# Kernel optimization log

Measured on AMD Instinct MI355X. Metric: run time of the kernel, lower is better.

## Reference

```python
import jax, jax.numpy as jnp
import numpy as np

N_NODES = 10000
N_EDGES = 640000
D_FEAT = 128
EPS = 1e-12  # F.normalize default eps


def setup_inputs() -> dict:
    key = jax.random.key(0)
    k1, k2, k3 = jax.random.split(key, 3)
    x = jax.random.normal(k1, (N_NODES, D_FEAT), dtype=jnp.float32)
    edge = jax.random.randint(k2, (3, N_EDGES), 0, N_NODES, dtype=jnp.int64)
    edge_weight = jax.random.uniform(k3, (N_EDGES,), dtype=jnp.float32)
    return {"x": x, "edge": edge, "edge_weight": edge_weight}


def reference(x, edge, edge_weight):
    edge_j = edge[0]  # source nodes
    edge_i = edge[2]  # target nodes
    n = x.shape[0]
    # degree of each target node (scatter_add of edge weights)
    deg = jax.ops.segment_sum(edge_weight, edge_i, num_segments=n)
    # normalized edge weights: w_e = ew_e / deg[target(e)]
    w = edge_weight / deg[edge_i]
    # SpMM: out[i] = sum_{e: target=i} w_e * x[source(e)]
    msg = x[edge_j] * w[:, None]           # [E, D]
    out = jax.ops.segment_sum(msg, edge_i, num_segments=n)  # [N, D]
    out = jax.nn.relu(out)
    # row-wise L2 normalize (F.normalize: x / max(||x||, eps))
    norm = jnp.sqrt(jnp.sum(out * out, axis=1, keepdims=True))
    return out / jnp.maximum(norm, EPS)
```

## Files before the change

kernel.cpp:

```cpp
#include <hip/hip_runtime.h>
#include <hip/hip_fp16.h>
#include <math.h>

#define D_FEAT 128
#define EPS 1e-12f
#define TGRP 40
#define NBUCK_PAD 256
#define NBLK 250
#define CAP_CB 40
#define SLOTS_PB (NBLK * CAP_CB)
#define LCAP 3584


__device__ inline float2 h2_to_f2(unsigned int u) {
    __half2 h = *reinterpret_cast<__half2*>(&u);
    return __half22float2(h);
}

__global__ __launch_bounds__(1024)
void build_kernel(const int* __restrict__ edge_i,
                  const int* __restrict__ edge_j,
                  const float* __restrict__ ew,
                  const float* __restrict__ x,
                  unsigned int* __restrict__ xh,
                  unsigned char* __restrict__ cntcb,
                  uint2* __restrict__ payload,
                  int E, int total4, int nbuck) {
    __shared__ unsigned int hc[NBUCK_PAD];
    const int c   = blockIdx.x;
    const int tid = threadIdx.x;
    const int EPB = E / NBLK;

    if (tid < NBUCK_PAD) hc[tid] = 0;
    __syncthreads();

    for (int i = c * 1024 + tid; i < total4; i += NBLK * 1024) {
        float4 v = ((const float4*)x)[i];
        __half2 h01 = __floats2half2_rn(v.x, v.y);
        __half2 h23 = __floats2half2_rn(v.z, v.w);
        uint2 o;
        o.x = *reinterpret_cast<unsigned int*>(&h01);
        o.y = *reinterpret_cast<unsigned int*>(&h23);
        ((uint2*)xh)[i] = o;
    }

    const int e0 = c * EPB;
    for (int k = tid; k < EPB; k += 1024) {
        int e = e0 + k;
        int t = edge_i[e];
        int bkt  = t / TGRP;
        int tloc = t - bkt * TGRP;
        unsigned int r = atomicAdd(&hc[bkt], 1u);
        if (r < CAP_CB) {
            unsigned short hw = __half_as_ushort(__float2half(ew[e]));
            payload[(size_t)bkt * SLOTS_PB + c * CAP_CB + r] =
                make_uint2(((unsigned int)edge_j[e] << 16) | (unsigned int)hw,
                           (unsigned int)tloc);
        }
    }
    __syncthreads();

    if (tid < nbuck) {
        unsigned int v = hc[tid];
        cntcb[(size_t)tid * NBUCK_PAD + c] =
            (unsigned char)(v > CAP_CB ? CAP_CB : v);
    }
}

__global__ __launch_bounds__(1024)
void sort_gather_kernel(const unsigned char* __restrict__ cntcb,
                        const uint2* __restrict__ payload,
                        const unsigned int* __restrict__ xh,
                        float* __restrict__ out, int n) {
    __shared__ unsigned char  cnt_c[NBLK];
    __shared__ unsigned int   cnt40[TGRP];
    __shared__ unsigned int   base40[TGRP + 1];
    __shared__ unsigned short rank16[SLOTS_PB];
    __shared__ unsigned int   ssw[LCAP];
    const int b   = blockIdx.x;
    const int tid = threadIdx.x;
    const int wv   = tid >> 6;
    const int lane = tid & 63;
    const int g    = lane >> 4;
    const int l16  = lane & 15;

    if (tid < NBLK) cnt_c[tid] = cntcb[(size_t)b * NBUCK_PAD + tid];
    if (tid < TGRP) cnt40[tid] = 0;
    __syncthreads();

    const uint2* __restrict__ pb = payload + (size_t)b * SLOTS_PB;

    for (int s = tid; s < SLOTS_PB; s += 1024) {
        uint2 pl = pb[s];
        int c = s / CAP_CB;
        int k = s - c * CAP_CB;
        if (k < (int)cnt_c[c]) {
            unsigned int r = atomicAdd(&cnt40[pl.y], 1u);
            rank16[s] = (unsigned short)r;
        }
    }
    __syncthreads();

    if (tid == 0) {
        unsigned int run = 0;
        for (int t = 0; t < TGRP; ++t) { base40[t] = run; run += cnt40[t]; }
        base40[TGRP] = run;
    }
    __syncthreads();

    for (int s = tid; s < SLOTS_PB; s += 1024) {
        uint2 pl = pb[s];
        int c = s / CAP_CB;
        int k = s - c * CAP_CB;
        if (k < (int)cnt_c[c]) {
            unsigned int pos = base40[pl.y] + (unsigned int)rank16[s];
            if (pos < LCAP) ssw[pos] = pl.x;
        }
    }
    __syncthreads();

    const uint4* __restrict__ xr = (const uint4*)xh;
    for (int tl = wv; tl < TGRP; tl += 16) {
        int t = b * TGRP + tl;
        if (t >= n) break;
        int beg = (int)base40[tl];
        int m   = (int)cnt40[tl];
        if (beg + m > LCAP) m = (LCAP - beg > 0) ? (LCAP - beg) : 0;

        float4 accA = {0.f,0.f,0.f,0.f};
        float4 accB = {0.f,0.f,0.f,0.f};

        int it = 0;
        for (; it + 15 < m; it += 16) {
            unsigned int pq[4]; uint4 hq[4];
            #pragma unroll
            for (int q = 0; q < 4; ++q) pq[q] = ssw[beg + it + q * 4 + g];
            #pragma unroll
            for (int q = 0; q < 4; ++q) hq[q] = xr[(size_t)(pq[q] >> 16) * 16 + l16];
            #pragma unroll
            for (int q = 0; q < 4; ++q) {
                float w = __half2float(__ushort_as_half((unsigned short)(pq[q] & 0xffffu)));
                float2 f;
                f = h2_to_f2(hq[q].x); accA.x = fmaf(f.x, w, accA.x); accA.y = fmaf(f.y, w, accA.y);
                f = h2_to_f2(hq[q].y); accA.z = fmaf(f.x, w, accA.z); accA.w = fmaf(f.y, w, accA.w);
                f = h2_to_f2(hq[q].z); accB.x = fmaf(f.x, w, accB.x); accB.y = fmaf(f.y, w, accB.y);
                f = h2_to_f2(hq[q].w); accB.z = fmaf(f.x, w, accB.z); accB.w = fmaf(f.y, w, accB.w);
            }
        }
        for (; it < m; it += 4) {
            int idx = it + g;
            unsigned int p = (idx < m) ? ssw[beg + idx] : 0u;
            uint4 h = xr[(size_t)(p >> 16) * 16 + l16];
            float w = __half2float(__ushort_as_half((unsigned short)(p & 0xffffu)));
            float2 f;
            f = h2_to_f2(h.x); accA.x = fmaf(f.x, w, accA.x); accA.y = fmaf(f.y, w, accA.y);
            f = h2_to_f2(h.y); accA.z = fmaf(f.x, w, accA.z); accA.w = fmaf(f.y, w, accA.w);
            f = h2_to_f2(h.z); accB.x = fmaf(f.x, w, accB.x); accB.y = fmaf(f.y, w, accB.y);
            f = h2_to_f2(h.w); accB.z = fmaf(f.x, w, accB.z); accB.w = fmaf(f.y, w, accB.w);
        }

        #pragma unroll
        for (int off = 16; off <= 32; off <<= 1) {
            accA.x += __shfl_xor(accA.x, off, 64);
            accA.y += __shfl_xor(accA.y, off, 64);
            accA.z += __shfl_xor(accA.z, off, 64);
            accA.w += __shfl_xor(accA.w, off, 64);
            accB.x += __shfl_xor(accB.x, off, 64);
            accB.y += __shfl_xor(accB.y, off, 64);
            accB.z += __shfl_xor(accB.z, off, 64);
            accB.w += __shfl_xor(accB.w, off, 64);
        }

        accA.x = fmaxf(accA.x, 0.f); accA.y = fmaxf(accA.y, 0.f);
        accA.z = fmaxf(accA.z, 0.f); accA.w = fmaxf(accA.w, 0.f);
        accB.x = fmaxf(accB.x, 0.f); accB.y = fmaxf(accB.y, 0.f);
        accB.z = fmaxf(accB.z, 0.f); accB.w = fmaxf(accB.w, 0.f);

        float ss = accA.x*accA.x + accA.y*accA.y + accA.z*accA.z + accA.w*accA.w
                 + accB.x*accB.x + accB.y*accB.y + accB.z*accB.z + accB.w*accB.w;
        #pragma unroll
        for (int off = 8; off > 0; off >>= 1) ss += __shfl_xor(ss, off, 64);

        float scale = 1.0f / fmaxf(sqrtf(ss), EPS);

        if (g == 0) {
            float4 o0 = { accA.x * scale, accA.y * scale, accA.z * scale, accA.w * scale };
            float4 o1 = { accB.x * scale, accB.y * scale, accB.z * scale, accB.w * scale };
            float4* orow = (float4*)out + (size_t)t * 32;
            orow[l16 * 2]     = o0;
            orow[l16 * 2 + 1] = o1;
        }
    }
}

__global__ void deg_kernel(const int* __restrict__ edge_i,
                           const float* __restrict__ ew,
                           float* __restrict__ deg, int E) {
    int e = blockIdx.x * blockDim.x + threadIdx.x;
    if (e < E) atomicAdd(&deg[edge_i[e]], ew[e]);
}

__global__ void scatter_kernel(const int* __restrict__ edge_j,
                               const int* __restrict__ edge_i,
                               const float* __restrict__ ew,
                               const float* __restrict__ deg,
                               const float* __restrict__ x,
                               float* __restrict__ out, int E) {
    int wave = (int)((blockIdx.x * (unsigned)blockDim.x + threadIdx.x) >> 6);
    int lane = threadIdx.x & 63;
    if (wave >= E) return;
    int tgt = edge_i[wave];
    int src = edge_j[wave];
    float w = ew[wave] / deg[tgt];
    const float2* xr = (const float2*)(x + (size_t)src * D_FEAT);
    float2 v = xr[lane];
    float* o = out + (size_t)tgt * D_FEAT + lane * 2;
    atomicAdd(o,     v.x * w);
    atomicAdd(o + 1, v.y * w);
}

__global__ void norm_kernel(float* __restrict__ out, int n) {
    int row = (int)((blockIdx.x * (unsigned)blockDim.x + threadIdx.x) >> 6);
    int lane = threadIdx.x & 63;
    if (row >= n) return;
    float2* o = (float2*)(out + (size_t)row * D_FEAT);
    float2 v = o[lane];
    v.x = fmaxf(v.x, 0.0f);
    v.y = fmaxf(v.y, 0.0f);
    float ss = v.x * v.x + v.y * v.y;
    #pragma unroll
    for (int off = 32; off > 0; off >>= 1) ss += __shfl_xor(ss, off, 64);
    float scale = 1.0f / fmaxf(sqrtf(ss), EPS);
    v.x *= scale;
    v.y *= scale;
    o[lane] = v;
}

static inline size_t align64(size_t v) { return (v + 63) & ~(size_t)63; }

extern "C" void kernel_launch(void* const* d_in, const int* in_sizes, int n_in,
                              void* d_out, int out_size, void* d_ws, size_t ws_size,
                              hipStream_t stream) {
    const float* x    = (const float*)d_in[0];
    const int*   edge = (const int*)d_in[1];
    const float* ew   = (const float*)d_in[2];
    float*       out  = (float*)d_out;

    const int E = in_sizes[2];
    const int n = in_sizes[0] / D_FEAT;

    const int* edge_j = edge;
    const int* edge_i = edge + 2 * (size_t)E;

    const int nbuck = (n + TGRP - 1) / TGRP;

    const size_t off_cnt = align64((size_t)n * D_FEAT * 2);
    const size_t off_pl  = align64(off_cnt + (size_t)nbuck * NBUCK_PAD);
    const size_t need    = off_pl + (size_t)nbuck * SLOTS_PB * 8;

    if (ws_size >= need && (E % NBLK) == 0 && nbuck <= NBLK &&
        (size_t)nbuck * TGRP >= (size_t)n && nbuck <= NBUCK_PAD) {
        char* ws = (char*)d_ws;
        unsigned int*  xh      = (unsigned int*)ws;
        unsigned char* cntcb   = (unsigned char*)(ws + off_cnt);
        uint2*         payload = (uint2*)(ws + off_pl);

        const int total4 = n * D_FEAT / 4;

        build_kernel<<<NBLK, 1024, 0, stream>>>(edge_i, edge_j, ew, x, xh,
                                                cntcb, payload, E, total4, nbuck);
        sort_gather_kernel<<<nbuck, 1024, 0, stream>>>(cntcb, payload, xh,
                                                       out, n);
    } else {
        float* deg = (float*)d_ws;
        hipMemsetAsync(deg, 0, (size_t)n * sizeof(float), stream);
        hipMemsetAsync(out, 0, (size_t)out_size * sizeof(float), stream);
        deg_kernel<<<(E + 255) / 256, 256, 0, stream>>>(edge_i, ew, deg, E);
        scatter_kernel<<<(E + 3) / 4, 256, 0, stream>>>(edge_j, edge_i, ew, deg, x, out, E);
        norm_kernel<<<(n + 3) / 4, 256, 0, stream>>>(out, n);
    }
}
```

Before: 88.85 us.

## Pack edge payload into 32 bits and compact slots in shared memory

Each edge payload shrinks from 8 bytes to 4 by packing a 14-bit source index, 6-bit local target and a 12-bit truncated fp16 weight, halving payload write and read traffic. The sort kernel no longer reads the padded payload slots twice from global memory. Valid entries are compacted into shared arrays in the first pass, and the scatter pass reads from LDS instead. The trade-off is reduced weight precision (rounded fp16 with 4 mantissa bits dropped), a new node-count limit of 16384, and more LDS use per block.

```diff
diff --git a/kernel.cpp b/kernel.cpp
--- a/kernel.cpp
+++ b/kernel.cpp
@@ -17,6 +17,10 @@
     return __half22float2(h);
 }
 
+__device__ inline float w12_to_f(unsigned int p) {
+    return __half2float(__ushort_as_half((unsigned short)((p & 0xfffu) << 4)));
+}
+
 __global__ __launch_bounds__(1024)
 void build_kernel(const int* __restrict__ edge_i,
                   const int* __restrict__ edge_j,
@@ -24,7 +28,7 @@
                   const float* __restrict__ x,
                   unsigned int* __restrict__ xh,
                   unsigned char* __restrict__ cntcb,
-                  uint2* __restrict__ payload,
+                  unsigned int* __restrict__ payload,
                   int E, int total4, int nbuck) {
     __shared__ unsigned int hc[NBUCK_PAD];
     const int c   = blockIdx.x;
@@ -52,10 +56,10 @@
         int tloc = t - bkt * TGRP;
         unsigned int r = atomicAdd(&hc[bkt], 1u);
         if (r < CAP_CB) {
-            unsigned short hw = __half_as_ushort(__float2half(ew[e]));
+            unsigned int hw = (unsigned int)__half_as_ushort(__float2half(ew[e]));
+            unsigned int w12 = (hw + 8u) >> 4;
             payload[(size_t)bkt * SLOTS_PB + c * CAP_CB + r] =
-                make_uint2(((unsigned int)edge_j[e] << 16) | (unsigned int)hw,
-                           (unsigned int)tloc);
+                ((unsigned int)edge_j[e] << 18) | ((unsigned int)tloc << 12) | w12;
         }
     }
     __syncthreads();
@@ -69,16 +73,18 @@
 
 __global__ __launch_bounds__(1024)
 void sort_gather_kernel(const unsigned char* __restrict__ cntcb,
-                        const uint2* __restrict__ payload,
+                        const unsigned int* __restrict__ payload,
                         const unsigned int* __restrict__ xh,
                         float* __restrict__ out, int n) {
-    __shared__ unsigned char  cnt_c[NBLK];
-    __shared__ unsigned int   cnt40[TGRP];
-    __shared__ unsigned int   base40[TGRP + 1];
-    __shared__ unsigned short rank16[SLOTS_PB];
-    __shared__ unsigned int   ssw[LCAP];
-    const int b   = blockIdx.x;
-    const int tid = threadIdx.x;
+    __shared__ unsigned char cnt_c[NBLK];
+    __shared__ unsigned int  cnt40[TGRP];
+    __shared__ unsigned int  base40[TGRP + 1];
+    __shared__ unsigned int  ccnt;
+    __shared__ unsigned int  lpl[LCAP];
+    __shared__ unsigned int  lpd[LCAP];
+    __shared__ unsigned int  ssw[LCAP];
+    const int b    = blockIdx.x;
+    const int tid  = threadIdx.x;
     const int wv   = tid >> 6;
     const int lane = tid & 63;
     const int g    = lane >> 4;
@@ -86,17 +92,23 @@
 
     if (tid < NBLK) cnt_c[tid] = cntcb[(size_t)b * NBUCK_PAD + tid];
     if (tid < TGRP) cnt40[tid] = 0;
-    __syncthreads();
-
-    const uint2* __restrict__ pb = payload + (size_t)b * SLOTS_PB;
+    if (tid == 0) ccnt = 0;
+    __syncthreads();
+
+    const unsigned int* __restrict__ pb = payload + (size_t)b * SLOTS_PB;
 
     for (int s = tid; s < SLOTS_PB; s += 1024) {
-        uint2 pl = pb[s];
+        unsigned int p = pb[s];
         int c = s / CAP_CB;
         int k = s - c * CAP_CB;
         if (k < (int)cnt_c[c]) {
-            unsigned int r = atomicAdd(&cnt40[pl.y], 1u);
-            rank16[s] = (unsigned short)r;
+            unsigned int tloc = (p >> 12) & 63u;
+            unsigned int r  = atomicAdd(&cnt40[tloc], 1u);
+            unsigned int ci = atomicAdd(&ccnt, 1u);
+            if (ci < LCAP) {
+                lpl[ci] = p;
+                lpd[ci] = (tloc << 16) | (r & 0xffffu);
+            }
         }
     }
     __syncthreads();
@@ -108,14 +120,12 @@
     }
     __syncthreads();
 
-    for (int s = tid; s < SLOTS_PB; s += 1024) {
-        uint2 pl = pb[s];
-        int c = s / CAP_CB;
-        int k = s - c * CAP_CB;
-        if (k < (int)cnt_c[c]) {
-            unsigned int pos = base40[pl.y] + (unsigned int)rank16[s];
-            if (pos < LCAP) ssw[pos] = pl.x;
-        }
+    unsigned int cc = ccnt;
+    if (cc > LCAP) cc = LCAP;
+    for (unsigned int i = tid; i < cc; i += 1024) {
+        unsigned int d = lpd[i];
+        unsigned int pos = base40[d >> 16] + (d & 0xffffu);
+        if (pos < LCAP) ssw[pos] = lpl[i];
     }
     __syncthreads();
 
@@ -136,10 +146,10 @@
             #pragma unroll
             for (int q = 0; q < 4; ++q) pq[q] = ssw[beg + it + q * 4 + g];
             #pragma unroll
-            for (int q = 0; q < 4; ++q) hq[q] = xr[(size_t)(pq[q] >> 16) * 16 + l16];
+            for (int q = 0; q < 4; ++q) hq[q] = xr[(size_t)(pq[q] >> 18) * 16 + l16];
             #pragma unroll
             for (int q = 0; q < 4; ++q) {
-                float w = __half2float(__ushort_as_half((unsigned short)(pq[q] & 0xffffu)));
+                float w = w12_to_f(pq[q]);
                 float2 f;
                 f = h2_to_f2(hq[q].x); accA.x = fmaf(f.x, w, accA.x); accA.y = fmaf(f.y, w, accA.y);
                 f = h2_to_f2(hq[q].y); accA.z = fmaf(f.x, w, accA.z); accA.w = fmaf(f.y, w, accA.w);
@@ -150,8 +160,8 @@
         for (; it < m; it += 4) {
             int idx = it + g;
             unsigned int p = (idx < m) ? ssw[beg + idx] : 0u;
-            uint4 h = xr[(size_t)(p >> 16) * 16 + l16];
-            float w = __half2float(__ushort_as_half((unsigned short)(p & 0xffffu)));
+            uint4 h = xr[(size_t)(p >> 18) * 16 + l16];
+            float w = w12_to_f(p);
             float2 f;
             f = h2_to_f2(h.x); accA.x = fmaf(f.x, w, accA.x); accA.y = fmaf(f.y, w, accA.y);
             f = h2_to_f2(h.y); accA.z = fmaf(f.x, w, accA.z); accA.w = fmaf(f.y, w, accA.w);
@@ -256,14 +266,14 @@
 
     const size_t off_cnt = align64((size_t)n * D_FEAT * 2);
     const size_t off_pl  = align64(off_cnt + (size_t)nbuck * NBUCK_PAD);
-    const size_t need    = off_pl + (size_t)nbuck * SLOTS_PB * 8;
+    const size_t need    = off_pl + (size_t)nbuck * SLOTS_PB * 4;
 
     if (ws_size >= need && (E % NBLK) == 0 && nbuck <= NBLK &&
-        (size_t)nbuck * TGRP >= (size_t)n && nbuck <= NBUCK_PAD) {
+        (size_t)nbuck * TGRP >= (size_t)n && nbuck <= NBUCK_PAD && n <= 16384) {
         char* ws = (char*)d_ws;
         unsigned int*  xh      = (unsigned int*)ws;
         unsigned char* cntcb   = (unsigned char*)(ws + off_cnt);
-        uint2*         payload = (uint2*)(ws + off_pl);
+        unsigned int*  payload = (unsigned int*)(ws + off_pl);
 
         const int total4 = n * D_FEAT / 4;
 
```

Result: faster. 87.01 us (-2.1%).
